# Performance work log

Hardware: AMD Instinct MI355X
Metric: run time of the kernel (lower is better)

The kernel has to match this reference:

```python
import jax, jax.numpy as jnp
import numpy as np

N_NODES = 100000

def setup_inputs() -> dict:
    key = jax.random.key(0)
    k1, k2, k3, k4 = jax.random.split(key, 4)
    E = 1600000
    x = jax.random.normal(k1, (N_NODES, 128), dtype=jnp.float32)
    src = jax.random.randint(k2, (E,), 0, N_NODES, dtype=jnp.int32)
    dst = jax.random.randint(k3, (E,), 0, N_NODES, dtype=jnp.int32)
    W = jax.random.normal(k4, (128, 128), dtype=jnp.float32) * (1.0 / np.sqrt(128.0))
    b = jnp.zeros((128,), dtype=jnp.float32)
    return {"x": x, "src": src, "dst": dst, "W": W, "b": b}

def reference(x, src, dst, W, b):
    # DGL GraphConv, norm='both', allow_zero_in_degree=True
    N = x.shape[0]
    ones = jnp.ones_like(src, dtype=x.dtype)
    out_deg = jax.ops.segment_sum(ones, src, num_segments=N)
    in_deg = jax.ops.segment_sum(ones, dst, num_segments=N)
    out_norm = jnp.power(jnp.clip(out_deg, 1.0), -0.5)  # [N]
    in_norm = jnp.power(jnp.clip(in_deg, 1.0), -0.5)    # [N]
    h = x * out_norm[:, None]                            # [N, d]
    msg = h[src]                                         # [E, d] gather
    agg = jax.ops.segment_sum(msg, dst, num_segments=N)  # [N, d] scatter-sum
    agg = agg * in_norm[:, None]
    return agg @ W + b
```

## Files before the change

kernel.cpp:

```cpp
#include <hip/hip_runtime.h>

#define NFEAT 128
#define BSHIFT 9
#define BNODES 512
#define NBMAX 256
#define CHUNK 4096

typedef __attribute__((ext_vector_type(8))) short bf16x8;
typedef __attribute__((ext_vector_type(4))) float f32x4;

__device__ inline unsigned short f2bf(float f) {
    unsigned u = __float_as_uint(f);
    u += 0x7FFF + ((u >> 16) & 1);
    return (unsigned short)(u >> 16);
}
__device__ inline float bf2f(unsigned short h) {
    return __uint_as_float((unsigned)h << 16);
}

__global__ __launch_bounds__(256)
void edge_count_kernel(const int* __restrict__ src, const int* __restrict__ dst, int E,
                       int* __restrict__ out_deg, int* __restrict__ bucket_cnt, int NB) {
    __shared__ int cnt[NBMAX];
    for (int i = threadIdx.x; i < NB; i += 256) cnt[i] = 0;
    __syncthreads();
    int base = blockIdx.x * CHUNK;
    int end = min(base + CHUNK, E);
    for (int j = base + threadIdx.x; j < end; j += 256) {
        atomicAdd(&out_deg[src[j]], 1);
        atomicAdd(&cnt[dst[j] >> BSHIFT], 1);
    }
    __syncthreads();
    for (int i = threadIdx.x; i < NB; i += 256)
        if (cnt[i]) atomicAdd(&bucket_cnt[i], cnt[i]);
}

__global__ void bucket_scan_kernel(const int* __restrict__ bucket_cnt,
                                   int* __restrict__ bucket_base,
                                   int* __restrict__ bucket_cursor, int NB) {
    __shared__ int sa[256], sb[256];
    int tid = threadIdx.x;
    int v = (tid < NB) ? bucket_cnt[tid] : 0;
    sa[tid] = v;
    __syncthreads();
    int* s = sa; int* t = sb;
    for (int d = 1; d < 256; d <<= 1) {
        t[tid] = s[tid] + (tid >= d ? s[tid - d] : 0);
        __syncthreads();
        int* tmp = s; s = t; t = tmp;
    }
    int incl = s[tid];
    int excl = incl - v;
    if (tid < NB) { bucket_base[tid] = excl; bucket_cursor[tid] = excl; }
    if (tid == 255) bucket_base[NB] = incl;
}

__global__ __launch_bounds__(256)
void partition_kernel(const int* __restrict__ src, const int* __restrict__ dst, int E,
                      int* __restrict__ bucket_cursor, int* __restrict__ packed, int NB) {
    __shared__ int cnt[NBMAX];
    for (int i = threadIdx.x; i < NB; i += 256) cnt[i] = 0;
    __syncthreads();
    int base = blockIdx.x * CHUNK;
    int end = min(base + CHUNK, E);
    for (int j = base + threadIdx.x; j < end; j += 256)
        atomicAdd(&cnt[dst[j] >> BSHIFT], 1);
    __syncthreads();
    for (int i = threadIdx.x; i < NB; i += 256) {
        int c = cnt[i];
        cnt[i] = c ? atomicAdd(&bucket_cursor[i], c) : 0;
    }
    __syncthreads();
    for (int j = base + threadIdx.x; j < end; j += 256) {
        int d = dst[j];
        int b = d >> BSHIFT;
        int pos = atomicAdd(&cnt[b], 1);
        packed[pos] = ((d & (BNODES - 1)) << 17) | src[j];
    }
}

__global__ __launch_bounds__(512)
void binfill_kernel(const int* __restrict__ packed, const int* __restrict__ bucket_base,
                    int* __restrict__ row_start, float* __restrict__ inorm,
                    int* __restrict__ csr_src, int N, int E) {
    __shared__ int cnt[BNODES];
    __shared__ int sa[BNODES], sb[BNODES];
    int bkt = blockIdx.x;
    int node0 = bkt << BSHIFT;
    int nn = min(BNODES, N - node0);
    int beg = bucket_base[bkt];
    int end = bucket_base[bkt + 1];
    int tid = threadIdx.x;

    cnt[tid] = 0;
    __syncthreads();
    for (int i = beg + tid; i < end; i += 512)
        atomicAdd(&cnt[packed[i] >> 17], 1);
    __syncthreads();

    int v = cnt[tid];
    sa[tid] = v;
    __syncthreads();
    int* s = sa; int* t = sb;
    for (int d = 1; d < 512; d <<= 1) {
        t[tid] = s[tid] + (tid >= d ? s[tid - d] : 0);
        __syncthreads();
        int* tmp = s; s = t; t = tmp;
    }
    int excl = s[tid] - v;

    if (tid < nn) {
        row_start[node0 + tid] = beg + excl;
        inorm[node0 + tid] = rsqrtf((float)max(v, 1));
    }
    if (bkt == 0 && tid == 0) row_start[N] = E;
    __syncthreads();

    cnt[tid] = beg + excl;
    __syncthreads();
    for (int i = beg + tid; i < end; i += 512) {
        int p = packed[i];
        int slot = atomicAdd(&cnt[p >> 17], 1);
        csr_src[slot] = p & 0x1FFFF;
    }
}


__global__ __launch_bounds__(256)
void cast_kernel(const float* __restrict__ x, const int* __restrict__ out_deg,
                 unsigned short* __restrict__ xh,
                 const float* __restrict__ W, unsigned short* __restrict__ Wt, int N) {
    int t = blockIdx.x * 256 + threadIdx.x;
    int total = N * (NFEAT / 4);
    if (t < total) {
        int row = t >> 5;
        float sc = rsqrtf((float)max(out_deg[row], 1));
        float4 v = reinterpret_cast<const float4*>(x)[t];
        ushort4 o;
        o.x = f2bf(v.x * sc); o.y = f2bf(v.y * sc);
        o.z = f2bf(v.z * sc); o.w = f2bf(v.w * sc);
        reinterpret_cast<ushort4*>(xh)[t] = o;
    } else {
        int i = t - total;
        if (i < NFEAT * NFEAT) {
            int col = i >> 7, k = i & 127;
            Wt[i] = f2bf(W[k * NFEAT + col]);
        }
    }
}

__global__ __launch_bounds__(256)
void agg_bf16_kernel(const unsigned short* __restrict__ xh, const int* __restrict__ csr_src,
                     const int* __restrict__ row_start, const float* __restrict__ inorm,
                     unsigned short* __restrict__ aggh, int N) {
    int node = blockIdx.x * 8 + (threadIdx.x >> 5);
    if (node >= N) return;
    int lf = threadIdx.x & 31;
    int beg = row_start[node];
    int end = row_start[node + 1];
    const ushort4* xr = reinterpret_cast<const ushort4*>(xh);

    float4 acc = make_float4(0.f, 0.f, 0.f, 0.f);
    for (int i = beg; i < end; i += 8) {
        int s[8];
        float m[8];
        #pragma unroll
        for (int u = 0; u < 8; ++u) {
            int j = i + u;
            bool ok = (j < end);
            s[u] = ok ? csr_src[j] : 0;
            m[u] = ok ? 1.f : 0.f;
        }
        ushort4 v[8];
        #pragma unroll
        for (int u = 0; u < 8; ++u) {
            v[u] = xr[s[u] * 32 + lf];
        }
        #pragma unroll
        for (int u = 0; u < 8; ++u) {
            acc.x = fmaf(m[u], bf2f(v[u].x), acc.x);
            acc.y = fmaf(m[u], bf2f(v[u].y), acc.y);
            acc.z = fmaf(m[u], bf2f(v[u].z), acc.z);
            acc.w = fmaf(m[u], bf2f(v[u].w), acc.w);
        }
    }
    float in_n = inorm[node];
    ushort4 o;
    o.x = f2bf(acc.x * in_n);
    o.y = f2bf(acc.y * in_n);
    o.z = f2bf(acc.z * in_n);
    o.w = f2bf(acc.w * in_n);
    *reinterpret_cast<ushort4*>(aggh + (size_t)node * 256 + lf * 4) = o;
}

__global__ __launch_bounds__(256)
void mm_mfma_kernel(const unsigned short* __restrict__ aggh, float* outp,
                    const unsigned short* __restrict__ Wt, const float* __restrict__ b, int N) {
    __shared__ unsigned short Al[NFEAT * NFEAT];
    __shared__ unsigned short Bl[NFEAT * NFEAT];
    int tid = threadIdx.x;
    int r0 = blockIdx.x * 128;

    for (int c = tid; c < 2048; c += 256) {
        int col = c >> 4, sub = c & 15;
        int slot = sub ^ (col & 7);
        *reinterpret_cast<uint4*>(reinterpret_cast<char*>(Bl) + col * 256 + slot * 16) =
            *reinterpret_cast<const uint4*>(reinterpret_cast<const char*>(Wt) + c * 16);
    }
    for (int c = tid; c < 2048; c += 256) {
        int row = c >> 4, sub = c & 15;
        int grow = min(r0 + row, N - 1);
        int slot = sub ^ (row & 7);
        *reinterpret_cast<uint4*>(reinterpret_cast<char*>(Al) + row * 256 + slot * 16) =
            *reinterpret_cast<const uint4*>(reinterpret_cast<const char*>(aggh) +
                                            (size_t)grow * 512 + sub * 16);
    }
    __syncthreads();

    int lane = tid & 63;
    int wave = tid >> 6;
    int wr = wave >> 1, wc = wave & 1;
    int lrow = lane & 15, hi = lane >> 4;

    f32x4 zero = {0.f, 0.f, 0.f, 0.f};
    f32x4 acc[4][4];
    #pragma unroll
    for (int rt = 0; rt < 4; ++rt)
        #pragma unroll
        for (int ct = 0; ct < 4; ++ct) acc[rt][ct] = zero;

    #pragma unroll
    for (int ks = 0; ks < 4; ++ks) {
        int chunk = ks * 4 + hi;
        bf16x8 af[4], bfr[4];
        #pragma unroll
        for (int rt = 0; rt < 4; ++rt) {
            int row = wr * 64 + rt * 16 + lrow;
            af[rt] = *reinterpret_cast<bf16x8*>(reinterpret_cast<char*>(Al) + row * 256 +
                                                ((chunk ^ (row & 7)) * 16));
        }
        #pragma unroll
        for (int ct = 0; ct < 4; ++ct) {
            int col = wc * 64 + ct * 16 + lrow;
            bfr[ct] = *reinterpret_cast<bf16x8*>(reinterpret_cast<char*>(Bl) + col * 256 +
                                                 ((chunk ^ (col & 7)) * 16));
        }
        #pragma unroll
        for (int rt = 0; rt < 4; ++rt)
            #pragma unroll
            for (int ct = 0; ct < 4; ++ct)
                acc[rt][ct] = __builtin_amdgcn_mfma_f32_16x16x32_bf16(af[rt], bfr[ct],
                                                                     acc[rt][ct], 0, 0, 0);
    }

    #pragma unroll
    for (int ct = 0; ct < 4; ++ct) {
        int col = wc * 64 + ct * 16 + lrow;
        float bias = b[col];
        #pragma unroll
        for (int rt = 0; rt < 4; ++rt) {
            int rbase = r0 + wr * 64 + rt * 16 + hi * 4;
            #pragma unroll
            for (int q = 0; q < 4; ++q) {
                int row = rbase + q;
                if (row < N) outp[(size_t)row * NFEAT + col] = acc[rt][ct][q] + bias;
            }
        }
    }
}


__global__ __launch_bounds__(256)
void agg_kernel(const float* __restrict__ x, const int* __restrict__ csr_src,
                const int* __restrict__ row_start, const int* __restrict__ out_deg,
                const float* __restrict__ inorm, float* __restrict__ out, int N) {
    int node = blockIdx.x * 8 + (threadIdx.x >> 5);
    if (node >= N) return;
    int lf = threadIdx.x & 31;
    int beg = row_start[node];
    int end = row_start[node + 1];

    float4 acc0 = make_float4(0.f, 0.f, 0.f, 0.f);
    float4 acc1 = make_float4(0.f, 0.f, 0.f, 0.f);
    int i = beg;
    for (; i + 1 < end; i += 2) {
        int s0 = csr_src[i];
        int s1 = csr_src[i + 1];
        float c0 = rsqrtf((float)max(out_deg[s0], 1));
        float c1 = rsqrtf((float)max(out_deg[s1], 1));
        float4 xv0 = *reinterpret_cast<const float4*>(&x[(size_t)s0 * NFEAT + lf * 4]);
        float4 xv1 = *reinterpret_cast<const float4*>(&x[(size_t)s1 * NFEAT + lf * 4]);
        acc0.x = fmaf(xv0.x, c0, acc0.x); acc0.y = fmaf(xv0.y, c0, acc0.y);
        acc0.z = fmaf(xv0.z, c0, acc0.z); acc0.w = fmaf(xv0.w, c0, acc0.w);
        acc1.x = fmaf(xv1.x, c1, acc1.x); acc1.y = fmaf(xv1.y, c1, acc1.y);
        acc1.z = fmaf(xv1.z, c1, acc1.z); acc1.w = fmaf(xv1.w, c1, acc1.w);
    }
    if (i < end) {
        int s0 = csr_src[i];
        float c0 = rsqrtf((float)max(out_deg[s0], 1));
        float4 xv0 = *reinterpret_cast<const float4*>(&x[(size_t)s0 * NFEAT + lf * 4]);
        acc0.x = fmaf(xv0.x, c0, acc0.x); acc0.y = fmaf(xv0.y, c0, acc0.y);
        acc0.z = fmaf(xv0.z, c0, acc0.z); acc0.w = fmaf(xv0.w, c0, acc0.w);
    }
    float in_n = inorm[node];
    float4 r;
    r.x = (acc0.x + acc1.x) * in_n;
    r.y = (acc0.y + acc1.y) * in_n;
    r.z = (acc0.z + acc1.z) * in_n;
    r.w = (acc0.w + acc1.w) * in_n;
    *reinterpret_cast<float4*>(&out[(size_t)node * NFEAT + lf * 4]) = r;
}

__global__ __launch_bounds__(512)
void mm_kernel(const float* agg, float* outp, const float* __restrict__ W,
               const float* __restrict__ b, int N) {
    __shared__ float Wl[NFEAT * NFEAT];

    for (int i = threadIdx.x; i < (NFEAT * NFEAT) / 4; i += 512) {
        reinterpret_cast<float4*>(Wl)[i] = reinterpret_cast<const float4*>(W)[i];
    }
    __syncthreads();

    const int wave = threadIdx.x >> 6;
    const int lane = threadIdx.x & 63;
    const int c0 = 2 * lane;
    const int r0 = (blockIdx.x * 8 + wave) * 8;
    if (r0 >= N) return;

    const float b0 = b[c0];
    const float b1 = b[c0 + 1];

    float acc[8][2];
    #pragma unroll
    for (int r = 0; r < 8; ++r) { acc[r][0] = b0; acc[r][1] = b1; }

    const float* arow = agg + (size_t)r0 * NFEAT;

    for (int k4 = 0; k4 < NFEAT; k4 += 4) {
        float4 a[8];
        #pragma unroll
        for (int r = 0; r < 8; ++r) {
            a[r] = *reinterpret_cast<const float4*>(arow + r * NFEAT + k4);
        }
        #pragma unroll
        for (int kk = 0; kk < 4; ++kk) {
            float2 w = *reinterpret_cast<const float2*>(&Wl[(k4 + kk) * NFEAT + c0]);
            #pragma unroll
            for (int r = 0; r < 8; ++r) {
                float av = (kk == 0) ? a[r].x : (kk == 1) ? a[r].y : (kk == 2) ? a[r].z : a[r].w;
                acc[r][0] = fmaf(av, w.x, acc[r][0]);
                acc[r][1] = fmaf(av, w.y, acc[r][1]);
            }
        }
    }

    #pragma unroll
    for (int r = 0; r < 8; ++r) {
        *reinterpret_cast<float2*>(&outp[(size_t)(r0 + r) * NFEAT + c0]) =
            make_float2(acc[r][0], acc[r][1]);
    }
}

extern "C" void kernel_launch(void* const* d_in, const int* in_sizes, int n_in,
                              void* d_out, int out_size, void* d_ws, size_t ws_size,
                              hipStream_t stream) {
    const float* x   = (const float*)d_in[0];
    const int*   src = (const int*)d_in[1];
    const int*   dst = (const int*)d_in[2];
    const float* W   = (const float*)d_in[3];
    const float* b   = (const float*)d_in[4];

    const int N = in_sizes[0] / NFEAT;
    const int E = in_sizes[1];
    float* out = (float*)d_out;

    const int NB = (N + BNODES - 1) >> BSHIFT;

    int*   out_deg       = (int*)d_ws;
    int*   bucket_cnt    = out_deg + N;
    int*   bucket_base   = bucket_cnt + NB;
    int*   bucket_cursor = bucket_base + (NB + 1);
    int*   row_start     = bucket_cursor + NB;
    float* inorm         = (float*)(row_start + (N + 1));
    int*   csr_src       = (int*)(inorm + N);
    unsigned short* Wt = (unsigned short*)(csr_src + E);
    unsigned short* xh = Wt + NFEAT * NFEAT;

    size_t need = (size_t)(csr_src + E - (int*)d_ws) * 4 +
                  (size_t)NFEAT * NFEAT * 2 + (size_t)N * NFEAT * 2;
    bool big = (ws_size >= need);

    int* packed = (int*)d_out;

    hipMemsetAsync(d_ws, 0, (size_t)(N + NB) * sizeof(int), stream);

    int nchunk = (E + CHUNK - 1) / CHUNK;
    edge_count_kernel<<<nchunk, 256, 0, stream>>>(src, dst, E, out_deg, bucket_cnt, NB);
    bucket_scan_kernel<<<1, 256, 0, stream>>>(bucket_cnt, bucket_base, bucket_cursor, NB);
    partition_kernel<<<nchunk, 256, 0, stream>>>(src, dst, E, bucket_cursor, packed, NB);
    binfill_kernel<<<NB, 512, 0, stream>>>(packed, bucket_base, row_start, inorm, csr_src, N, E);

    if (big) {
        int cast_threads = N * 32 + NFEAT * NFEAT;
        cast_kernel<<<(cast_threads + 255) / 256, 256, 0, stream>>>(x, out_deg, xh, W, Wt, N);
        unsigned short* aggh = (unsigned short*)d_out;
        agg_bf16_kernel<<<(N + 7) / 8, 256, 0, stream>>>(xh, csr_src, row_start, inorm, aggh, N);
        mm_mfma_kernel<<<(N + 127) / 128, 256, 0, stream>>>(aggh, out, Wt, b, N);
    } else {
        agg_kernel<<<(N + 7) / 8, 256, 0, stream>>>(x, csr_src, row_start, out_deg, inorm, out, N);
        mm_kernel<<<(N + 63) / 64, 512, 0, stream>>>(out, out, W, b, N);
    }
}
```

Measured before the change: 242.3 us.

## Slice bf16 features into 8 column-major slabs for cache-local gather aggregation

The cast kernel now writes the normalized bf16 features into 8 separate slabs of 16 features per node, transposing them through LDS. The aggregation kernel assigns each block one slab for 64 nodes, so the gathered working set per slab (about 3.2 MB) can stay resident in L2 instead of the full 25.6 MB table. The fp32 fallback path and the workspace-size check are removed, and the packed edge buffer moves to the tail of the output buffer. Each edge index is now loaded 8 times (once per slice), and each gather is only 32 bytes per node, which costs extra index traffic and smaller memory transactions.

```diff
diff --git a/kernel.cpp b/kernel.cpp
--- a/kernel.cpp
+++ b/kernel.cpp
@@ -5,16 +5,19 @@
 #define BNODES 512
 #define NBMAX 256
 #define CHUNK 4096
+#define NSLICE 8
+#define SFEAT 16
 
 typedef __attribute__((ext_vector_type(8))) short bf16x8;
 typedef __attribute__((ext_vector_type(4))) float f32x4;
-
-__device__ inline unsigned short f2bf(float f) {
+typedef unsigned short u16;
+
+__device__ inline u16 f2bf(float f) {
     unsigned u = __float_as_uint(f);
     u += 0x7FFF + ((u >> 16) & 1);
-    return (unsigned short)(u >> 16);
-}
-__device__ inline float bf2f(unsigned short h) {
+    return (u16)(u >> 16);
+}
+__device__ inline float bf2f(u16 h) {
     return __uint_as_float((unsigned)h << 16);
 }
 
@@ -125,79 +128,97 @@
     }
 }
 
-
 __global__ __launch_bounds__(256)
 void cast_kernel(const float* __restrict__ x, const int* __restrict__ out_deg,
-                 unsigned short* __restrict__ xh,
-                 const float* __restrict__ W, unsigned short* __restrict__ Wt, int N) {
-    int t = blockIdx.x * 256 + threadIdx.x;
-    int total = N * (NFEAT / 4);
-    if (t < total) {
-        int row = t >> 5;
-        float sc = rsqrtf((float)max(out_deg[row], 1));
-        float4 v = reinterpret_cast<const float4*>(x)[t];
+                 u16* __restrict__ xh_s, const float* __restrict__ W,
+                 u16* __restrict__ Wt, int N, int NBLK) {
+    int bid = blockIdx.x;
+    int tid = threadIdx.x;
+    if (bid == NBLK) {
+        for (int i = tid; i < NFEAT * NFEAT; i += 256) {
+            int col = i >> 7, k = i & 127;
+            Wt[i] = f2bf(W[k * NFEAT + col]);
+        }
+        return;
+    }
+    __shared__ u16 lds[64][136];
+    int node0 = bid << 6;
+    for (int i = tid; i < 64 * 32; i += 256) {
+        int row = i >> 5, f4 = i & 31;
+        int n = node0 + row;
+        float4 v = make_float4(0.f, 0.f, 0.f, 0.f);
+        float sc = 0.f;
+        if (n < N) {
+            v = *reinterpret_cast<const float4*>(&x[(size_t)n * NFEAT + f4 * 4]);
+            sc = rsqrtf((float)max(out_deg[n], 1));
+        }
         ushort4 o;
         o.x = f2bf(v.x * sc); o.y = f2bf(v.y * sc);
         o.z = f2bf(v.z * sc); o.w = f2bf(v.w * sc);
-        reinterpret_cast<ushort4*>(xh)[t] = o;
-    } else {
-        int i = t - total;
-        if (i < NFEAT * NFEAT) {
-            int col = i >> 7, k = i & 127;
-            Wt[i] = f2bf(W[k * NFEAT + col]);
-        }
-    }
-}
-
-__global__ __launch_bounds__(256)
-void agg_bf16_kernel(const unsigned short* __restrict__ xh, const int* __restrict__ csr_src,
-                     const int* __restrict__ row_start, const float* __restrict__ inorm,
-                     unsigned short* __restrict__ aggh, int N) {
-    int node = blockIdx.x * 8 + (threadIdx.x >> 5);
-    if (node >= N) return;
-    int lf = threadIdx.x & 31;
-    int beg = row_start[node];
-    int end = row_start[node + 1];
-    const ushort4* xr = reinterpret_cast<const ushort4*>(xh);
+        *reinterpret_cast<ushort4*>(&lds[row][f4 * 4]) = o;
+    }
+    __syncthreads();
+    int nn = tid >> 2, f4 = tid & 3;
+    int n = node0 + nn;
+    if (n < N) {
+        #pragma unroll
+        for (int s = 0; s < NSLICE; ++s) {
+            ushort4 o = *reinterpret_cast<ushort4*>(&lds[nn][s * SFEAT + f4 * 4]);
+            *reinterpret_cast<ushort4*>(&xh_s[((size_t)s * N + n) * SFEAT + f4 * 4]) = o;
+        }
+    }
+}
+
+__global__ __launch_bounds__(256)
+void agg_sliced_kernel(const u16* __restrict__ xh_s, const int* __restrict__ csr_src,
+                       const int* __restrict__ row_start, const float* __restrict__ inorm,
+                       u16* __restrict__ aggh, int N) {
+    int bid = blockIdx.x;
+    int s = bid & 7;
+    int node0 = (bid >> 3) << 6;
+    int g = threadIdx.x >> 2;
+    int l4 = threadIdx.x & 3;
+    int n = node0 + g;
+    if (n >= N) return;
+    int beg = row_start[n];
+    int end = row_start[n + 1];
+    const ushort4* base = reinterpret_cast<const ushort4*>(xh_s + (size_t)s * N * SFEAT);
 
     float4 acc = make_float4(0.f, 0.f, 0.f, 0.f);
     for (int i = beg; i < end; i += 8) {
-        int s[8];
-        float m[8];
+        int idx[8]; float mk[8];
         #pragma unroll
         for (int u = 0; u < 8; ++u) {
             int j = i + u;
             bool ok = (j < end);
-            s[u] = ok ? csr_src[j] : 0;
-            m[u] = ok ? 1.f : 0.f;
+            idx[u] = ok ? csr_src[j] : 0;
+            mk[u] = ok ? 1.f : 0.f;
         }
         ushort4 v[8];
         #pragma unroll
+        for (int u = 0; u < 8; ++u)
+            v[u] = base[(size_t)idx[u] * 4 + l4];
+        #pragma unroll
         for (int u = 0; u < 8; ++u) {
-            v[u] = xr[s[u] * 32 + lf];
-        }
-        #pragma unroll
-        for (int u = 0; u < 8; ++u) {
-            acc.x = fmaf(m[u], bf2f(v[u].x), acc.x);
-            acc.y = fmaf(m[u], bf2f(v[u].y), acc.y);
-            acc.z = fmaf(m[u], bf2f(v[u].z), acc.z);
-            acc.w = fmaf(m[u], bf2f(v[u].w), acc.w);
-        }
-    }
-    float in_n = inorm[node];
+            acc.x = fmaf(mk[u], bf2f(v[u].x), acc.x);
+            acc.y = fmaf(mk[u], bf2f(v[u].y), acc.y);
+            acc.z = fmaf(mk[u], bf2f(v[u].z), acc.z);
+            acc.w = fmaf(mk[u], bf2f(v[u].w), acc.w);
+        }
+    }
+    float sc = inorm[n];
     ushort4 o;
-    o.x = f2bf(acc.x * in_n);
-    o.y = f2bf(acc.y * in_n);
-    o.z = f2bf(acc.z * in_n);
-    o.w = f2bf(acc.w * in_n);
-    *reinterpret_cast<ushort4*>(aggh + (size_t)node * 256 + lf * 4) = o;
-}
-
-__global__ __launch_bounds__(256)
-void mm_mfma_kernel(const unsigned short* __restrict__ aggh, float* outp,
-                    const unsigned short* __restrict__ Wt, const float* __restrict__ b, int N) {
-    __shared__ unsigned short Al[NFEAT * NFEAT];
-    __shared__ unsigned short Bl[NFEAT * NFEAT];
+    o.x = f2bf(acc.x * sc); o.y = f2bf(acc.y * sc);
+    o.z = f2bf(acc.z * sc); o.w = f2bf(acc.w * sc);
+    *reinterpret_cast<ushort4*>(reinterpret_cast<char*>(aggh) +
+                                (size_t)n * 512 + s * 32 + l4 * 8) = o;
+}
+
+__global__ __launch_bounds__(256)
+void mm_mfma_kernel(const u16* __restrict__ aggh, float* outp,
+                    const u16* __restrict__ Wt, const float* __restrict__ b, int N) {
+    __shared__ u16 Al[NFEAT * NFEAT];
+    __shared__ u16 Bl[NFEAT * NFEAT];
     int tid = threadIdx.x;
     int r0 = blockIdx.x * 128;
 
@@ -266,98 +287,6 @@
                 if (row < N) outp[(size_t)row * NFEAT + col] = acc[rt][ct][q] + bias;
             }
         }
-    }
-}
-
-
-__global__ __launch_bounds__(256)
-void agg_kernel(const float* __restrict__ x, const int* __restrict__ csr_src,
-                const int* __restrict__ row_start, const int* __restrict__ out_deg,
-                const float* __restrict__ inorm, float* __restrict__ out, int N) {
-    int node = blockIdx.x * 8 + (threadIdx.x >> 5);
-    if (node >= N) return;
-    int lf = threadIdx.x & 31;
-    int beg = row_start[node];
-    int end = row_start[node + 1];
-
-    float4 acc0 = make_float4(0.f, 0.f, 0.f, 0.f);
-    float4 acc1 = make_float4(0.f, 0.f, 0.f, 0.f);
-    int i = beg;
-    for (; i + 1 < end; i += 2) {
-        int s0 = csr_src[i];
-        int s1 = csr_src[i + 1];
-        float c0 = rsqrtf((float)max(out_deg[s0], 1));
-        float c1 = rsqrtf((float)max(out_deg[s1], 1));
-        float4 xv0 = *reinterpret_cast<const float4*>(&x[(size_t)s0 * NFEAT + lf * 4]);
-        float4 xv1 = *reinterpret_cast<const float4*>(&x[(size_t)s1 * NFEAT + lf * 4]);
-        acc0.x = fmaf(xv0.x, c0, acc0.x); acc0.y = fmaf(xv0.y, c0, acc0.y);
-        acc0.z = fmaf(xv0.z, c0, acc0.z); acc0.w = fmaf(xv0.w, c0, acc0.w);
-        acc1.x = fmaf(xv1.x, c1, acc1.x); acc1.y = fmaf(xv1.y, c1, acc1.y);
-        acc1.z = fmaf(xv1.z, c1, acc1.z); acc1.w = fmaf(xv1.w, c1, acc1.w);
-    }
-    if (i < end) {
-        int s0 = csr_src[i];
-        float c0 = rsqrtf((float)max(out_deg[s0], 1));
-        float4 xv0 = *reinterpret_cast<const float4*>(&x[(size_t)s0 * NFEAT + lf * 4]);
-        acc0.x = fmaf(xv0.x, c0, acc0.x); acc0.y = fmaf(xv0.y, c0, acc0.y);
-        acc0.z = fmaf(xv0.z, c0, acc0.z); acc0.w = fmaf(xv0.w, c0, acc0.w);
-    }
-    float in_n = inorm[node];
-    float4 r;
-    r.x = (acc0.x + acc1.x) * in_n;
-    r.y = (acc0.y + acc1.y) * in_n;
-    r.z = (acc0.z + acc1.z) * in_n;
-    r.w = (acc0.w + acc1.w) * in_n;
-    *reinterpret_cast<float4*>(&out[(size_t)node * NFEAT + lf * 4]) = r;
-}
-
-__global__ __launch_bounds__(512)
-void mm_kernel(const float* agg, float* outp, const float* __restrict__ W,
-               const float* __restrict__ b, int N) {
-    __shared__ float Wl[NFEAT * NFEAT];
-
-    for (int i = threadIdx.x; i < (NFEAT * NFEAT) / 4; i += 512) {
-        reinterpret_cast<float4*>(Wl)[i] = reinterpret_cast<const float4*>(W)[i];
-    }
-    __syncthreads();
-
-    const int wave = threadIdx.x >> 6;
-    const int lane = threadIdx.x & 63;
-    const int c0 = 2 * lane;
-    const int r0 = (blockIdx.x * 8 + wave) * 8;
-    if (r0 >= N) return;
-
-    const float b0 = b[c0];
-    const float b1 = b[c0 + 1];
-
-    float acc[8][2];
-    #pragma unroll
-    for (int r = 0; r < 8; ++r) { acc[r][0] = b0; acc[r][1] = b1; }
-
-    const float* arow = agg + (size_t)r0 * NFEAT;
-
-    for (int k4 = 0; k4 < NFEAT; k4 += 4) {
-        float4 a[8];
-        #pragma unroll
-        for (int r = 0; r < 8; ++r) {
-            a[r] = *reinterpret_cast<const float4*>(arow + r * NFEAT + k4);
-        }
-        #pragma unroll
-        for (int kk = 0; kk < 4; ++kk) {
-            float2 w = *reinterpret_cast<const float2*>(&Wl[(k4 + kk) * NFEAT + c0]);
-            #pragma unroll
-            for (int r = 0; r < 8; ++r) {
-                float av = (kk == 0) ? a[r].x : (kk == 1) ? a[r].y : (kk == 2) ? a[r].z : a[r].w;
-                acc[r][0] = fmaf(av, w.x, acc[r][0]);
-                acc[r][1] = fmaf(av, w.y, acc[r][1]);
-            }
-        }
-    }
-
-    #pragma unroll
-    for (int r = 0; r < 8; ++r) {
-        *reinterpret_cast<float2*>(&outp[(size_t)(r0 + r) * NFEAT + c0]) =
-            make_float2(acc[r][0], acc[r][1]);
     }
 }
 
@@ -378,36 +307,31 @@
 
     int*   out_deg       = (int*)d_ws;
     int*   bucket_cnt    = out_deg + N;
-    int*   bucket_base   = bucket_cnt + NB;
-    int*   bucket_cursor = bucket_base + (NB + 1);
-    int*   row_start     = bucket_cursor + NB;
+    int*   bucket_base   = bucket_cnt + NBMAX;
+    int*   bucket_cursor = bucket_base + (NBMAX + 1);
+    int*   row_start     = bucket_cursor + NBMAX;
     float* inorm         = (float*)(row_start + (N + 1));
     int*   csr_src       = (int*)(inorm + N);
-    unsigned short* Wt = (unsigned short*)(csr_src + E);
-    unsigned short* xh = Wt + NFEAT * NFEAT;
-
-    size_t need = (size_t)(csr_src + E - (int*)d_ws) * 4 +
-                  (size_t)NFEAT * NFEAT * 2 + (size_t)N * NFEAT * 2;
-    bool big = (ws_size >= need);
-
-    int* packed = (int*)d_out;
-
-    hipMemsetAsync(d_ws, 0, (size_t)(N + NB) * sizeof(int), stream);
+    u16*   Wt            = (u16*)(csr_src + E);
+    u16*   xh_s          = Wt + NFEAT * NFEAT;
+
+    int* packed = (int*)((char*)d_out + (size_t)out_size * 4 - (size_t)E * 4);
+
+    hipMemsetAsync(d_ws, 0, (size_t)(N + NBMAX) * sizeof(int), stream);
 
     int nchunk = (E + CHUNK - 1) / CHUNK;
     edge_count_kernel<<<nchunk, 256, 0, stream>>>(src, dst, E, out_deg, bucket_cnt, NB);
     bucket_scan_kernel<<<1, 256, 0, stream>>>(bucket_cnt, bucket_base, bucket_cursor, NB);
     partition_kernel<<<nchunk, 256, 0, stream>>>(src, dst, E, bucket_cursor, packed, NB);
-    binfill_kernel<<<NB, 512, 0, stream>>>(packed, bucket_base, row_start, inorm, csr_src, N, E);
-
-    if (big) {
-        int cast_threads = N * 32 + NFEAT * NFEAT;
-        cast_kernel<<<(cast_threads + 255) / 256, 256, 0, stream>>>(x, out_deg, xh, W, Wt, N);
-        unsigned short* aggh = (unsigned short*)d_out;
-        agg_bf16_kernel<<<(N + 7) / 8, 256, 0, stream>>>(xh, csr_src, row_start, inorm, aggh, N);
-        mm_mfma_kernel<<<(N + 127) / 128, 256, 0, stream>>>(aggh, out, Wt, b, N);
-    } else {
-        agg_kernel<<<(N + 7) / 8, 256, 0, stream>>>(x, csr_src, row_start, out_deg, inorm, out, N);
-        mm_kernel<<<(N + 63) / 64, 512, 0, stream>>>(out, out, W, b, N);
-    }
-}
+    binfill_kernel<<<NB, 512, 0, stream>>>(packed, bucket_base, row_start, inorm,
+                                           csr_src, N, E);
+
+    int nb64 = (N + 63) >> 6;
+    cast_kernel<<<nb64 + 1, 256, 0, stream>>>(x, out_deg, xh_s, W, Wt, N, nb64);
+
+    u16* aggh = (u16*)d_out;
+    agg_sliced_kernel<<<nb64 * NSLICE, 256, 0, stream>>>(xh_s, csr_src, row_start,
+                                                         inorm, aggh, N);
+
+    mm_mfma_kernel<<<(N + 127) / 128, 256, 0, stream>>>(aggh, out, Wt, b, N);
+}
```

Result: slower. 281.1 us (+16.0%).
